# Kernel tuning notes

Measured on AMD Instinct MI355X. Metric: run time of the kernel, lower is better.

## Reference

```python
import jax, jax.numpy as jnp
import numpy as np

B, N, C, H, D, K = 4, 8192, 384, 12, 2, 256
M = N // K          # 32 members per cluster
CH = C // H         # 32 head dim


def setup_inputs() -> dict:
    key = jax.random.key(0)
    ks = jax.random.split(key, 8)
    pos = jax.random.uniform(ks[0], (B, N, D), jnp.float32) * 100.0
    feat = jax.random.normal(ks[1], (B, N, C), jnp.float32)
    # each batch's points partitioned into K clusters of M members (a permutation)
    perms = jax.vmap(lambda kk: jax.random.permutation(kk, N))(jax.random.split(ks[2], B))
    member_idx = perms.reshape(B * K, M).astype(jnp.int32)               # z x m
    batch_idx = jnp.broadcast_to(
        jnp.repeat(jnp.arange(B, dtype=jnp.int32), K)[:, None], (B * K, M))
    w = 0.02
    qkv_w = jax.random.normal(ks[3], (3 * C, C), jnp.float32) * w
    qkv_b = jnp.zeros((3 * C,), jnp.float32)
    pos_w = jax.random.normal(ks[4], (H, D), jnp.float32) * w
    pos_b = jnp.zeros((H,), jnp.float32)
    proj_w = jax.random.normal(ks[5], (C, C), jnp.float32) * w
    proj_b = jnp.zeros((C,), jnp.float32)
    return dict(pos=pos, feat=feat, member_idx=member_idx, batch_idx=batch_idx,
                qkv_w=qkv_w, qkv_b=qkv_b, pos_w=pos_w, pos_b=pos_b,
                proj_w=proj_w, proj_b=proj_b, k=K)


def reference(pos, feat, member_idx, batch_idx, qkv_w, qkv_b, pos_w, pos_b,
              proj_w, proj_b, k):
    # attend_means=True, mask=None, cluster_score=None, q_subsample_idx=None path
    b, n, c = feat.shape
    d = pos.shape[2]
    h = pos_w.shape[0]
    ch = c // h
    z, m = member_idx.shape
    scale = ch ** -0.5

    qkv = feat @ qkv_w.T + qkv_b            # b,n,3c
    q = qkv[..., :c]                        # b,n,c
    kv = qkv[..., c:]                       # b,n,2c

    pos_orig = pos
    pos_n = pos / jnp.max(pos.reshape(-1, d), axis=0)   # per-coordinate max norm

    # irregular gather of kv / pos per cluster member
    kv_g = kv[batch_idx, member_idx]        # z,m,2c
    pos_g = pos_n[batch_idx, member_idx]    # z,m,d

    # cluster_score=None, mask=None -> uniform weights 1/m (mean over members)
    kv_mean = jnp.mean(kv_g, axis=1).reshape(b, k, 2, h, ch)
    pos_mean = jnp.mean(pos_g, axis=1).reshape(b, k, d)

    key_ = kv_mean[:, :, 0].transpose(0, 2, 1, 3)   # b,h,k,ch
    v = kv_mean[:, :, 1].transpose(0, 2, 1, 3)      # b,h,k,ch
    qh = q.reshape(b, n, h, ch).transpose(0, 2, 1, 3) * scale  # b,h,n,ch

    attn = jnp.einsum('bhnc,bhkc->bhnk', qh, key_)  # b,h,n,k
    rel_pos = pos_mean[:, None, :, :] - pos_orig[:, :, None, :]  # b,n,k,d
    pos_bias = jnp.einsum('bnkd,hd->bhnk', rel_pos, pos_w) + pos_b[None, :, None, None]
    attn = jax.nn.softmax(attn + pos_bias, axis=-1)

    out = jnp.einsum('bhnk,bhkc->bnhc', attn, v).reshape(b, n, c)
    return out @ proj_w.T + proj_b
```

## Files before the change

### kernel.cpp

```cpp
#include <hip/hip_runtime.h>

typedef __attribute__((ext_vector_type(8))) short bf16x8;
typedef __attribute__((ext_vector_type(4))) float f32x4;

#define MFMA16(a,b,c) __builtin_amdgcn_mfma_f32_16x16x32_bf16((a),(b),(c),0,0,0)

__device__ __forceinline__ float b2f(unsigned short u){
  union { unsigned u; float f; } x; x.u = ((unsigned)u) << 16; return x.f;
}
__device__ __forceinline__ unsigned short f2b(float f){
  union { float f; unsigned u; } x; x.f = f;
  unsigned r = x.u + 0x7FFFu + ((x.u >> 16) & 1u);
  return (unsigned short)(r >> 16);
}
__device__ __forceinline__ unsigned pk_rne(float a, float b){
  unsigned ua = __float_as_uint(a), ub = __float_as_uint(b);
  ua += 0x7FFFu + ((ua >> 16) & 1u);
  ub += 0x7FFFu + ((ub >> 16) & 1u);
  return __builtin_amdgcn_perm(ub, ua, 0x07060302u);
}
__device__ __forceinline__ unsigned pk_trunc(float a, float b){
  return __builtin_amdgcn_perm(__float_as_uint(b), __float_as_uint(a), 0x07060302u);
}
__device__ __forceinline__ bf16x8 mk8(unsigned a, unsigned b, unsigned c, unsigned d){
  union { uint4 u; bf16x8 h; } x; x.u = make_uint4(a,b,c,d); return x.h;
}
__device__ __forceinline__ int permp(int cl){
  return (cl & 0xE0) | (((cl >> 2) & 3) << 3) | (((cl >> 4) & 1) << 2) | (cl & 3);
}

typedef __attribute__((address_space(3))) unsigned int lds_u32;
typedef const __attribute__((address_space(1))) unsigned int glb_u32;
__device__ __forceinline__ void gl_lds16(const void* g, void* l){
  __builtin_amdgcn_global_load_lds((glb_u32*)g, (lds_u32*)l, 16, 0, 0);
}

__global__ __launch_bounds__(256) void cvt_kernel(const float* __restrict__ in,
                                                  unsigned short* __restrict__ o, long n8){
  long i = (long)blockIdx.x*256 + threadIdx.x;
  if (i >= n8) return;
  const float4* p = (const float4*)(in + i*8);
  float4 a = p[0], b = p[1];
  *(uint4*)(o + i*8) = make_uint4(pk_rne(a.x,a.y), pk_rne(a.z,a.w),
                                  pk_rne(b.x,b.y), pk_rne(b.z,b.w));
}

__global__ __launch_bounds__(256) void posmax_kernel(const float* __restrict__ pos,
                                                     unsigned* __restrict__ pmax){
  int i = blockIdx.x*256 + threadIdx.x;
  float4 v = ((const float4*)pos)[i];
  float m0 = fmaxf(v.x, v.z), m1 = fmaxf(v.y, v.w);
  #pragma unroll
  for (int off = 32; off >= 1; off >>= 1){
    m0 = fmaxf(m0, __shfl_xor(m0, off, 64));
    m1 = fmaxf(m1, __shfl_xor(m1, off, 64));
  }
  if ((threadIdx.x & 63) == 0){
    atomicMax(&pmax[0], __float_as_uint(m0));
    atomicMax(&pmax[1], __float_as_uint(m1));
  }
}

__global__ __launch_bounds__(192) void cluster_means_kernel(
    const float* __restrict__ feat, const float* __restrict__ pos,
    const int* __restrict__ member_idx, const int* __restrict__ batch_idx,
    unsigned short* __restrict__ fm, float* __restrict__ pm)
{
  int t = threadIdx.x;
  int g = t / 96, tl = t - g*96;
  int z = blockIdx.x*2 + g;
  __shared__ int bases[2][32];
  if (tl < 32) bases[g][tl] = batch_idx[z*32 + tl]*8192 + member_idx[z*32 + tl];
  __syncthreads();
  float4 a = {0.f,0.f,0.f,0.f};
  float p = 0.f;
  const float4* f4 = (const float4*)feat;
  #pragma unroll 4
  for (int m = 0; m < 32; m++){
    int row = bases[g][m];
    float4 v = f4[(long)row*96 + tl];
    a.x += v.x; a.y += v.y; a.z += v.z; a.w += v.w;
    if (tl < 2) p += pos[(long)row*2 + tl];
  }
  unsigned d0 = pk_rne(a.x*(1.f/32.f), a.y*(1.f/32.f));
  unsigned d1 = pk_rne(a.z*(1.f/32.f), a.w*(1.f/32.f));
  *(uint2*)(fm + (long)z*384 + tl*4) = make_uint2(d0, d1);
  if (tl < 2) pm[z*2 + tl] = p * (1.f/32.f);
}

__global__ __launch_bounds__(256) void bias_kernel(
    const float* __restrict__ pm, const float* __restrict__ pmaxf,
    const float* __restrict__ pos_w, const float* __restrict__ pos_b,
    unsigned short* __restrict__ wt)
{
  int idx = blockIdx.x*256 + threadIdx.x;
  int kc = idx & 255;
  int bh = idx >> 8;
  int h = bh % 12;
  float p0 = pm[((bh/12)*256 + kc)*2]   / pmaxf[0];
  float p1 = pm[((bh/12)*256 + kc)*2+1] / pmaxf[1];
  float bias = p0*pos_w[h*2] + p1*pos_w[h*2+1] + pos_b[h];
  wt[(bh << 8) + permp(kc)] = f2b(exp2f(bias * 1.44269504088896340f));
}

__global__ __launch_bounds__(256) void gemm_kv_kernel(
    const unsigned short* __restrict__ A, const unsigned short* __restrict__ W,
    const float* __restrict__ bias, unsigned short* __restrict__ kh,
    unsigned short* __restrict__ vt, const unsigned short* __restrict__ wt)
{
  __shared__ unsigned short As[64*64];
  __shared__ unsigned short Ws[128*64];
  const int N = 768, K = 384;
  int mt = blockIdx.x / 6, nt = blockIdx.x - mt*6;
  int m0 = mt << 6, n0 = nt << 7;
  int tid = threadIdx.x;
  int lane = tid & 63, wave = tid >> 6;
  int wr = (wave >> 1) << 5, wc = (wave & 1) << 6;
  int l15 = lane & 15, quad = lane >> 4;
  int sw = l15 & 7;
  int srow = tid >> 3, sc8 = tid & 7;

  f32x4 acc[2][4];
  #pragma unroll
  for (int i = 0; i < 2; i++)
    #pragma unroll
    for (int j = 0; j < 4; j++) acc[i][j] = (f32x4){0.f,0.f,0.f,0.f};

  for (int k0 = 0; k0 < K; k0 += 64){
    __syncthreads();
    #pragma unroll
    for (int it = 0; it < 2; it++){
      int r = srow + it*32;
      int gc8 = sc8 ^ (r & 7);
      gl_lds16(A + (long)(m0+r)*K + k0 + gc8*8, As + it*2048 + wave*512);
    }
    #pragma unroll
    for (int it = 0; it < 4; it++){
      int r = srow + it*32;
      int gc8 = sc8 ^ (r & 7);
      gl_lds16(W + (long)(n0+r)*K + k0 + gc8*8, Ws + it*2048 + wave*512);
    }
    __syncthreads();
    #pragma unroll
    for (int kk = 0; kk < 2; kk++){
      bf16x8 af[2], bfr[4];
      #pragma unroll
      for (int i = 0; i < 2; i++)
        af[i] = *(const bf16x8*)(As + (wr + i*16 + l15)*64 + (((kk<<2)+quad) ^ sw)*8);
      #pragma unroll
      for (int j = 0; j < 4; j++)
        bfr[j] = *(const bf16x8*)(Ws + (wc + j*16 + l15)*64 + (((kk<<2)+quad) ^ sw)*8);
      #pragma unroll
      for (int i = 0; i < 2; i++)
        #pragma unroll
        for (int j = 0; j < 4; j++)
          acc[i][j] = MFMA16(af[i], bfr[j], acc[i][j]);
    }
  }

  #pragma unroll
  for (int j = 0; j < 4; j++){
    int col = n0 + wc + j*16 + l15;
    float bv = bias[col];
    #pragma unroll
    for (int i = 0; i < 2; i++){
      int row0 = m0 + wr + i*16 + quad*4;
      #pragma unroll
      for (int r = 0; r < 4; r++){
        float v = acc[i][j][r] + bv;
        int row = row0 + r;
        int b = row >> 8, cl = row & 255;
        if (col < 384){
          int h = col >> 5, ch = col & 31;
          kh[((((long)b*12 + h)*256 + cl)*32) + ch] = f2b(v);
        } else {
          int cn = col - 384;
          int h = cn >> 5, ch = cn & 31;
          int pp = permp(cl);
          int c8 = (pp >> 3) ^ (ch & 7);
          float w = b2f(wt[(((long)b*12 + h) << 8) + pp]);
          vt[(((long)b*12 + h)*32 + ch)*256 + c8*8 + (pp & 7)] = f2b(v * w);
        }
      }
    }
  }
}

template<int OUT_F32, int AF32>
__global__ __launch_bounds__(512) void gemm_fn_kernel(
    const void* __restrict__ Av, const unsigned short* __restrict__ W,
    const float* __restrict__ bias, void* __restrict__ Cv, float out_scale)
{
  __shared__ unsigned short As[64*72];
  __shared__ unsigned short Ws[384*64];
  const int K = 384, N = 384;
  int m0 = blockIdx.x << 6;
  int tid = threadIdx.x;
  int lane = tid & 63, wave = tid >> 6;
  int l15 = lane & 15, quad = lane >> 4;
  int sw = l15 & 7;
  int srow = tid >> 3, sc8 = tid & 7;

  f32x4 acc[4][3];
  #pragma unroll
  for (int i = 0; i < 4; i++)
    #pragma unroll
    for (int j = 0; j < 3; j++) acc[i][j] = (f32x4){0.f,0.f,0.f,0.f};

  for (int k0 = 0; k0 < K; k0 += 64){
    __syncthreads();
    if (AF32){
      const float* Af = (const float*)Av;
      const float4* src = (const float4*)(Af + (long)(m0+srow)*K + k0 + sc8*8);
      float4 v0 = src[0], v1 = src[1];
      *(uint4*)(As + srow*72 + sc8*8) = make_uint4(pk_rne(v0.x,v0.y), pk_rne(v0.z,v0.w),
                                                   pk_rne(v1.x,v1.y), pk_rne(v1.z,v1.w));
    } else {
      const unsigned short* A = (const unsigned short*)Av;
      int gc8 = sc8 ^ (srow & 7);
      gl_lds16(A + (long)(m0+srow)*K + k0 + gc8*8, As + wave*512);
    }
    #pragma unroll
    for (int it = 0; it < 6; it++){
      int r = it*64 + srow;
      int gc8 = sc8 ^ (r & 7);
      gl_lds16(W + (long)r*K + k0 + gc8*8, Ws + it*4096 + wave*512);
    }
    __syncthreads();
    #pragma unroll
    for (int kk = 0; kk < 2; kk++){
      bf16x8 af[4];
      #pragma unroll
      for (int i = 0; i < 4; i++){
        int r = i*16 + l15;
        if (AF32) af[i] = *(const bf16x8*)(As + r*72 + ((kk<<2)+quad)*8);
        else      af[i] = *(const bf16x8*)(As + r*64 + (((kk<<2)+quad) ^ sw)*8);
      }
      #pragma unroll
      for (int j = 0; j < 3; j++){
        bf16x8 bfr = *(const bf16x8*)(Ws + (wave*48 + j*16 + l15)*64 + (((kk<<2)+quad) ^ sw)*8);
        #pragma unroll
        for (int i = 0; i < 4; i++)
          acc[i][j] = MFMA16(af[i], bfr, acc[i][j]);
      }
    }
  }

  #pragma unroll
  for (int j = 0; j < 3; j++){
    int col = wave*48 + j*16 + l15;
    float bv = bias[col];
    #pragma unroll
    for (int i = 0; i < 4; i++){
      int row0 = m0 + i*16 + quad*4;
      #pragma unroll
      for (int r = 0; r < 4; r++){
        float v = (acc[i][j][r] + bv) * out_scale;
        if (OUT_F32) ((float*)Cv)[(long)(row0+r)*N + col] = v;
        else ((unsigned short*)Cv)[(long)(row0+r)*N + col] = f2b(v);
      }
    }
  }
}

__global__ __launch_bounds__(256) void attn_kernel(
    const unsigned short* __restrict__ qs,
    const unsigned short* __restrict__ kh,
    const unsigned short* __restrict__ vt,
    const unsigned short* __restrict__ wt,
    unsigned short* __restrict__ ao)
{
  __shared__ unsigned short keyS[256*32];
  __shared__ unsigned short vTS[32*256];
  __shared__ unsigned short wS[256];

  int bid = blockIdx.x;
  int chunk = bid & 127;
  int h = (bid >> 7) % 12;
  int b = bid / (128*12);
  int bh = b*12 + h;
  int n0 = chunk << 6;
  int tid = threadIdx.x, lane = tid & 63, wave = tid >> 6;
  int l15 = lane & 15, quad = lane >> 4;
  int sw = l15 & 7;

  const unsigned short* khb = kh + (long)bh*8192;
  const unsigned short* vtb = vt + (long)bh*8192;
  #pragma unroll
  for (int it = 0; it < 4; it++){
    gl_lds16(khb + it*2048 + tid*8, keyS + it*2048 + wave*512);
    gl_lds16(vtb + it*2048 + tid*8, vTS  + it*2048 + wave*512);
  }
  if (tid < 32) *(uint4*)(wS + tid*8) = *(const uint4*)(wt + ((long)bh << 8) + tid*8);
  __syncthreads();

  int tok0 = n0 + wave*16;
  bf16x8 aq = *(const bf16x8*)(qs + ((long)b*8192 + tok0 + l15)*384 + h*32 + quad*8);

  f32x4 S[16];
  #pragma unroll
  for (int kb = 0; kb < 16; kb++){
    bf16x8 bk = *(const bf16x8*)(keyS + (kb*16 + l15)*32 + quad*8);
    f32x4 z = {0.f,0.f,0.f,0.f};
    S[kb] = MFMA16(bk, aq, z);
  }

  #pragma unroll
  for (int kb = 0; kb < 16; kb++)
    #pragma unroll
    for (int c = 0; c < 4; c++) S[kb][c] = exp2f(S[kb][c]);

  f32x4 o0 = {0.f,0.f,0.f,0.f}, o1 = {0.f,0.f,0.f,0.f}, os = {0.f,0.f,0.f,0.f};
  #pragma unroll
  for (int ks = 0; ks < 8; ks++){
    bf16x8 pf = mk8(pk_trunc(S[2*ks][0],   S[2*ks][1]),
                    pk_trunc(S[2*ks][2],   S[2*ks][3]),
                    pk_trunc(S[2*ks+1][0], S[2*ks+1][1]),
                    pk_trunc(S[2*ks+1][2], S[2*ks+1][3]));
    int c8 = (4*ks + quad) ^ sw;
    bf16x8 a0 = *(const bf16x8*)(vTS + l15*256      + c8*8);
    bf16x8 a1 = *(const bf16x8*)(vTS + (16+l15)*256 + c8*8);
    bf16x8 wf = *(const bf16x8*)(wS + ks*32 + quad*8);
    o0 = MFMA16(a0, pf, o0);
    o1 = MFMA16(a1, pf, o1);
    os = MFMA16(wf, pf, os);
  }
  float inv = 1.f / os[0];
  long obase = ((long)b*8192 + tok0 + l15)*384 + h*32 + quad*4;
  unsigned q0 = pk_rne(o0[0]*inv, o0[1]*inv), q1 = pk_rne(o0[2]*inv, o0[3]*inv);
  unsigned q2 = pk_rne(o1[0]*inv, o1[1]*inv), q3 = pk_rne(o1[2]*inv, o1[3]*inv);
  *(uint2*)(ao + obase)      = make_uint2(q0, q1);
  *(uint2*)(ao + obase + 16) = make_uint2(q2, q3);
}

extern "C" void kernel_launch(void* const* d_in, const int* in_sizes, int n_in,
                              void* d_out, int out_size, void* d_ws, size_t ws_size,
                              hipStream_t stream)
{
  const float* pos      = (const float*)d_in[0];
  const float* feat     = (const float*)d_in[1];
  const int* member_idx = (const int*)d_in[2];
  const int* batch_idx  = (const int*)d_in[3];
  const float* qkv_w    = (const float*)d_in[4];
  const float* qkv_b    = (const float*)d_in[5];
  const float* pos_w    = (const float*)d_in[6];
  const float* pos_b    = (const float*)d_in[7];
  const float* proj_w   = (const float*)d_in[8];
  const float* proj_b   = (const float*)d_in[9];
  float* out = (float*)d_out;

  char* ws = (char*)d_ws;
  float* pmax           = (float*)ws;
  float* pm             = (float*)(ws + 256);
  unsigned short* fm    = (unsigned short*)(ws + 8704);
  unsigned short* kh    = (unsigned short*)(ws + 795136);
  unsigned short* vt    = (unsigned short*)(ws + 1581568);
  unsigned short* wt    = (unsigned short*)(ws + 2368000);
  unsigned short* q_s   = (unsigned short*)(ws + 2417152);
  unsigned short* ao    = (unsigned short*)(ws + 27582976);
  unsigned short* qkvwb = (unsigned short*)(ws + 52748800);
  unsigned short* projwb= (unsigned short*)(ws + 53633536);

  hipMemsetAsync(pmax, 0, 8, stream);
  posmax_kernel<<<64, 256, 0, stream>>>(pos, (unsigned*)pmax);
  cvt_kernel<<<216, 256, 0, stream>>>(qkv_w, qkvwb, 55296);
  cvt_kernel<<<72, 256, 0, stream>>>(proj_w, projwb, 18432);
  cluster_means_kernel<<<512, 192, 0, stream>>>(feat, pos, member_idx, batch_idx, fm, pm);
  bias_kernel<<<48, 256, 0, stream>>>(pm, pmax, pos_w, pos_b, wt);
  gemm_kv_kernel<<<96, 256, 0, stream>>>(fm, qkvwb + 384*384, qkv_b + 384, kh, vt, wt);
  gemm_fn_kernel<0,1><<<512, 512, 0, stream>>>(feat, qkvwb, qkv_b, q_s,
                                               0.17677669529663687f * 1.44269504088896340f);
  attn_kernel<<<6144, 256, 0, stream>>>(q_s, kh, vt, wt, ao);
  gemm_fn_kernel<1,0><<<512, 512, 0, stream>>>(ao, projwb, proj_b, out, 1.0f);
}
```

Measured before the change: 224.8 us.

## Fuse prep kernels and restructure row GEMM to read weights from global

Merges the position-max reduction and the two weight-conversion kernels into one launch to save launch overhead. The row GEMM now stages the whole 64x384 A tile in LDS once and reads B fragments directly from global memory (L2-resident bf16 weights) instead of staging 384x64 weight slices each k-step. This drops the per-k-step barriers and cuts LDS use, which may raise occupancy. The cost is more global/L2 traffic per wave for the weight fragments. The cluster-means loop unroll also goes from 4 to 8.

```diff
diff --git a/kernel.cpp b/kernel.cpp
--- a/kernel.cpp
+++ b/kernel.cpp
@@ -35,29 +35,33 @@
   __builtin_amdgcn_global_load_lds((glb_u32*)g, (lds_u32*)l, 16, 0, 0);
 }
 
-__global__ __launch_bounds__(256) void cvt_kernel(const float* __restrict__ in,
-                                                  unsigned short* __restrict__ o, long n8){
-  long i = (long)blockIdx.x*256 + threadIdx.x;
-  if (i >= n8) return;
-  const float4* p = (const float4*)(in + i*8);
-  float4 a = p[0], b = p[1];
-  *(uint4*)(o + i*8) = make_uint4(pk_rne(a.x,a.y), pk_rne(a.z,a.w),
-                                  pk_rne(b.x,b.y), pk_rne(b.z,b.w));
-}
-
-__global__ __launch_bounds__(256) void posmax_kernel(const float* __restrict__ pos,
-                                                     unsigned* __restrict__ pmax){
-  int i = blockIdx.x*256 + threadIdx.x;
-  float4 v = ((const float4*)pos)[i];
-  float m0 = fmaxf(v.x, v.z), m1 = fmaxf(v.y, v.w);
-  #pragma unroll
-  for (int off = 32; off >= 1; off >>= 1){
-    m0 = fmaxf(m0, __shfl_xor(m0, off, 64));
-    m1 = fmaxf(m1, __shfl_xor(m1, off, 64));
-  }
-  if ((threadIdx.x & 63) == 0){
-    atomicMax(&pmax[0], __float_as_uint(m0));
-    atomicMax(&pmax[1], __float_as_uint(m1));
+__global__ __launch_bounds__(256) void prep_kernel(
+    const float* __restrict__ pos, unsigned* __restrict__ pmax,
+    const float* __restrict__ qkv_w, unsigned short* __restrict__ qkvwb,
+    const float* __restrict__ proj_w, unsigned short* __restrict__ projwb)
+{
+  int bid = blockIdx.x, tid = threadIdx.x;
+  if (bid < 64){
+    int i = bid*256 + tid;
+    float4 v = ((const float4*)pos)[i];
+    float m0 = fmaxf(v.x, v.z), m1 = fmaxf(v.y, v.w);
+    #pragma unroll
+    for (int off = 32; off >= 1; off >>= 1){
+      m0 = fmaxf(m0, __shfl_xor(m0, off, 64));
+      m1 = fmaxf(m1, __shfl_xor(m1, off, 64));
+    }
+    if ((tid & 63) == 0){
+      atomicMax(&pmax[0], __float_as_uint(m0));
+      atomicMax(&pmax[1], __float_as_uint(m1));
+    }
+  } else {
+    const float* in; unsigned short* o; long i;
+    if (bid < 280){ in = qkv_w;  o = qkvwb;  i = (long)(bid-64)*256 + tid; }
+    else          { in = proj_w; o = projwb; i = (long)(bid-280)*256 + tid; }
+    const float4* p = (const float4*)(in + i*8);
+    float4 a = p[0], b = p[1];
+    *(uint4*)(o + i*8) = make_uint4(pk_rne(a.x,a.y), pk_rne(a.z,a.w),
+                                    pk_rne(b.x,b.y), pk_rne(b.z,b.w));
   }
 }
 
@@ -75,7 +79,7 @@
   float4 a = {0.f,0.f,0.f,0.f};
   float p = 0.f;
   const float4* f4 = (const float4*)feat;
-  #pragma unroll 4
+  #pragma unroll 8
   for (int m = 0; m < 32; m++){
     int row = bases[g][m];
     float4 v = f4[(long)row*96 + tl];
@@ -191,15 +195,33 @@
     const void* __restrict__ Av, const unsigned short* __restrict__ W,
     const float* __restrict__ bias, void* __restrict__ Cv, float out_scale)
 {
-  __shared__ unsigned short As[64*72];
-  __shared__ unsigned short Ws[384*64];
+  __shared__ unsigned short As[6*64*64];
   const int K = 384, N = 384;
   int m0 = blockIdx.x << 6;
   int tid = threadIdx.x;
   int lane = tid & 63, wave = tid >> 6;
   int l15 = lane & 15, quad = lane >> 4;
-  int sw = l15 & 7;
-  int srow = tid >> 3, sc8 = tid & 7;
+  int sr = tid >> 3, sc8 = tid & 7;
+
+  if (AF32){
+    const float* Af = (const float*)Av;
+    #pragma unroll
+    for (int it = 0; it < 6; it++){
+      int gc = it*64 + (sc8 ^ (sr & 7))*8;
+      const float4* src = (const float4*)(Af + (long)(m0+sr)*K + gc);
+      float4 v0 = src[0], v1 = src[1];
+      *(uint4*)(As + it*4096 + sr*64 + sc8*8) =
+        make_uint4(pk_rne(v0.x,v0.y), pk_rne(v0.z,v0.w), pk_rne(v1.x,v1.y), pk_rne(v1.z,v1.w));
+    }
+  } else {
+    const unsigned short* A = (const unsigned short*)Av;
+    #pragma unroll
+    for (int it = 0; it < 6; it++){
+      int gc8 = sc8 ^ (sr & 7);
+      gl_lds16(A + (long)(m0+sr)*K + it*64 + gc8*8, As + it*4096 + wave*512);
+    }
+  }
+  __syncthreads();
 
   f32x4 acc[4][3];
   #pragma unroll
@@ -207,48 +229,29 @@
     #pragma unroll
     for (int j = 0; j < 3; j++) acc[i][j] = (f32x4){0.f,0.f,0.f,0.f};
 
-  for (int k0 = 0; k0 < K; k0 += 64){
-    __syncthreads();
-    if (AF32){
-      const float* Af = (const float*)Av;
-      const float4* src = (const float4*)(Af + (long)(m0+srow)*K + k0 + sc8*8);
-      float4 v0 = src[0], v1 = src[1];
-      *(uint4*)(As + srow*72 + sc8*8) = make_uint4(pk_rne(v0.x,v0.y), pk_rne(v0.z,v0.w),
-                                                   pk_rne(v1.x,v1.y), pk_rne(v1.z,v1.w));
-    } else {
-      const unsigned short* A = (const unsigned short*)Av;
-      int gc8 = sc8 ^ (srow & 7);
-      gl_lds16(A + (long)(m0+srow)*K + k0 + gc8*8, As + wave*512);
-    }
-    #pragma unroll
-    for (int it = 0; it < 6; it++){
-      int r = it*64 + srow;
-      int gc8 = sc8 ^ (r & 7);
-      gl_lds16(W + (long)r*K + k0 + gc8*8, Ws + it*4096 + wave*512);
-    }
-    __syncthreads();
-    #pragma unroll
-    for (int kk = 0; kk < 2; kk++){
-      bf16x8 af[4];
-      #pragma unroll
-      for (int i = 0; i < 4; i++){
-        int r = i*16 + l15;
-        if (AF32) af[i] = *(const bf16x8*)(As + r*72 + ((kk<<2)+quad)*8);
-        else      af[i] = *(const bf16x8*)(As + r*64 + (((kk<<2)+quad) ^ sw)*8);
-      }
-      #pragma unroll
-      for (int j = 0; j < 3; j++){
-        bf16x8 bfr = *(const bf16x8*)(Ws + (wave*48 + j*16 + l15)*64 + (((kk<<2)+quad) ^ sw)*8);
-        #pragma unroll
-        for (int i = 0; i < 4; i++)
-          acc[i][j] = MFMA16(af[i], bfr, acc[i][j]);
-      }
-    }
+  int n0w = wave*48;
+  #pragma unroll
+  for (int ks = 0; ks < 12; ks++){
+    int it = ks >> 1, cb = (ks & 1)*4;
+    bf16x8 af[4], bw[3];
+    #pragma unroll
+    for (int j = 0; j < 3; j++)
+      bw[j] = *(const bf16x8*)(W + (long)(n0w + j*16 + l15)*K + ks*32 + quad*8);
+    #pragma unroll
+    for (int i = 0; i < 4; i++){
+      int r = i*16 + l15;
+      af[i] = *(const bf16x8*)(As + it*4096 + r*64 + (((cb+quad) ^ (l15 & 7))*8));
+    }
+    #pragma unroll
+    for (int i = 0; i < 4; i++)
+      #pragma unroll
+      for (int j = 0; j < 3; j++)
+        acc[i][j] = MFMA16(af[i], bw[j], acc[i][j]);
   }
 
   #pragma unroll
   for (int j = 0; j < 3; j++){
-    int col = wave*48 + j*16 + l15;
+    int col = n0w + j*16 + l15;
     float bv = bias[col];
     #pragma unroll
     for (int i = 0; i < 4; i++){
@@ -362,9 +365,7 @@
   unsigned short* projwb= (unsigned short*)(ws + 53633536);
 
   hipMemsetAsync(pmax, 0, 8, stream);
-  posmax_kernel<<<64, 256, 0, stream>>>(pos, (unsigned*)pmax);
-  cvt_kernel<<<216, 256, 0, stream>>>(qkv_w, qkvwb, 55296);
-  cvt_kernel<<<72, 256, 0, stream>>>(proj_w, projwb, 18432);
+  prep_kernel<<<352, 256, 0, stream>>>(pos, (unsigned*)pmax, qkv_w, qkvwb, proj_w, projwb);
   cluster_means_kernel<<<512, 192, 0, stream>>>(feat, pos, member_idx, batch_idx, fm, pm);
   bias_kernel<<<48, 256, 0, stream>>>(pm, pmax, pos_w, pos_b, wt);
   gemm_kv_kernel<<<96, 256, 0, stream>>>(fm, qkvwb + 384*384, qkv_b + 384, kh, vt, wt);
```

Result: slower. 238.7 us (+6.2%).

## Use head-major Q and attention-output layouts, double attention work per block, fuse prep kernels

Applied to the files above, without the earlier changes.

The Q projection now writes its output in head-major (b,h,n,32) layout, and the output projection reads attention output from that layout. This gives the attention kernel contiguous 64-byte rows per token instead of strided 384-wide rows. Each attention block now handles 128 tokens (two 16-token tiles per wave), so key/value staging is amortized over twice the work and the grid is halved. The pos-max and two weight-conversion kernels are merged into one launch, and the cluster-means loop unroll is raised. The cost is scattered 2-byte stores in the Q GEMM epilogue and gathered loads in the proj GEMM, plus fewer blocks in the attention grid.

```diff
diff --git a/kernel.cpp b/kernel.cpp
--- a/kernel.cpp
+++ b/kernel.cpp
@@ -35,29 +35,33 @@
   __builtin_amdgcn_global_load_lds((glb_u32*)g, (lds_u32*)l, 16, 0, 0);
 }
 
-__global__ __launch_bounds__(256) void cvt_kernel(const float* __restrict__ in,
-                                                  unsigned short* __restrict__ o, long n8){
-  long i = (long)blockIdx.x*256 + threadIdx.x;
-  if (i >= n8) return;
-  const float4* p = (const float4*)(in + i*8);
-  float4 a = p[0], b = p[1];
-  *(uint4*)(o + i*8) = make_uint4(pk_rne(a.x,a.y), pk_rne(a.z,a.w),
-                                  pk_rne(b.x,b.y), pk_rne(b.z,b.w));
-}
-
-__global__ __launch_bounds__(256) void posmax_kernel(const float* __restrict__ pos,
-                                                     unsigned* __restrict__ pmax){
-  int i = blockIdx.x*256 + threadIdx.x;
-  float4 v = ((const float4*)pos)[i];
-  float m0 = fmaxf(v.x, v.z), m1 = fmaxf(v.y, v.w);
-  #pragma unroll
-  for (int off = 32; off >= 1; off >>= 1){
-    m0 = fmaxf(m0, __shfl_xor(m0, off, 64));
-    m1 = fmaxf(m1, __shfl_xor(m1, off, 64));
-  }
-  if ((threadIdx.x & 63) == 0){
-    atomicMax(&pmax[0], __float_as_uint(m0));
-    atomicMax(&pmax[1], __float_as_uint(m1));
+__global__ __launch_bounds__(256) void prep_kernel(
+    const float* __restrict__ pos, unsigned* __restrict__ pmax,
+    const float* __restrict__ qkv_w, unsigned short* __restrict__ qkvwb,
+    const float* __restrict__ proj_w, unsigned short* __restrict__ projwb)
+{
+  int bid = blockIdx.x, tid = threadIdx.x;
+  if (bid < 64){
+    int i = bid*256 + tid;
+    float4 v = ((const float4*)pos)[i];
+    float m0 = fmaxf(v.x, v.z), m1 = fmaxf(v.y, v.w);
+    #pragma unroll
+    for (int off = 32; off >= 1; off >>= 1){
+      m0 = fmaxf(m0, __shfl_xor(m0, off, 64));
+      m1 = fmaxf(m1, __shfl_xor(m1, off, 64));
+    }
+    if ((tid & 63) == 0){
+      atomicMax(&pmax[0], __float_as_uint(m0));
+      atomicMax(&pmax[1], __float_as_uint(m1));
+    }
+  } else {
+    const float* in; unsigned short* o; long i;
+    if (bid < 280){ in = qkv_w;  o = qkvwb;  i = (long)(bid-64)*256 + tid; }
+    else          { in = proj_w; o = projwb; i = (long)(bid-280)*256 + tid; }
+    const float4* p = (const float4*)(in + i*8);
+    float4 a = p[0], b = p[1];
+    *(uint4*)(o + i*8) = make_uint4(pk_rne(a.x,a.y), pk_rne(a.z,a.w),
+                                    pk_rne(b.x,b.y), pk_rne(b.z,b.w));
   }
 }
 
@@ -75,7 +79,7 @@
   float4 a = {0.f,0.f,0.f,0.f};
   float p = 0.f;
   const float4* f4 = (const float4*)feat;
-  #pragma unroll 4
+  #pragma unroll 8
   for (int m = 0; m < 32; m++){
     int row = bases[g][m];
     float4 v = f4[(long)row*96 + tl];
@@ -186,7 +190,7 @@
   }
 }
 
-template<int OUT_F32, int AF32>
+template<int OUT_F32, int AF32, int AHM, int CHM>
 __global__ __launch_bounds__(512) void gemm_fn_kernel(
     const void* __restrict__ Av, const unsigned short* __restrict__ W,
     const float* __restrict__ bias, void* __restrict__ Cv, float out_scale)
@@ -218,7 +222,16 @@
     } else {
       const unsigned short* A = (const unsigned short*)Av;
       int gc8 = sc8 ^ (srow & 7);
-      gl_lds16(A + (long)(m0+srow)*K + k0 + gc8*8, As + wave*512);
+      const unsigned short* src;
+      if (AHM){
+        int row = m0 + srow;
+        int bb = row >> 13, tok = row & 8191;
+        int ch = k0 + gc8*8;
+        src = A + ((((long)(bb*12 + (ch >> 5))) << 13) + tok)*32 + (ch & 31);
+      } else {
+        src = A + (long)(m0+srow)*K + k0 + gc8*8;
+      }
+      gl_lds16(src, As + wave*512);
     }
     #pragma unroll
     for (int it = 0; it < 6; it++){
@@ -256,30 +269,35 @@
       #pragma unroll
       for (int r = 0; r < 4; r++){
         float v = (acc[i][j][r] + bv) * out_scale;
-        if (OUT_F32) ((float*)Cv)[(long)(row0+r)*N + col] = v;
-        else ((unsigned short*)Cv)[(long)(row0+r)*N + col] = f2b(v);
+        int row = row0 + r;
+        if (OUT_F32){
+          ((float*)Cv)[(long)row*N + col] = v;
+        } else if (CHM){
+          int bb = row >> 13, tok = row & 8191;
+          ((unsigned short*)Cv)[((((long)(bb*12 + (col >> 5))) << 13) + tok)*32 + (col & 31)] = f2b(v);
+        } else {
+          ((unsigned short*)Cv)[(long)row*N + col] = f2b(v);
+        }
       }
     }
   }
 }
 
 __global__ __launch_bounds__(256) void attn_kernel(
-    const unsigned short* __restrict__ qs,
+    const unsigned short* __restrict__ qhm,
     const unsigned short* __restrict__ kh,
     const unsigned short* __restrict__ vt,
     const unsigned short* __restrict__ wt,
-    unsigned short* __restrict__ ao)
+    unsigned short* __restrict__ aohm)
 {
   __shared__ unsigned short keyS[256*32];
   __shared__ unsigned short vTS[32*256];
   __shared__ unsigned short wS[256];
 
   int bid = blockIdx.x;
-  int chunk = bid & 127;
-  int h = (bid >> 7) % 12;
-  int b = bid / (128*12);
-  int bh = b*12 + h;
-  int n0 = chunk << 6;
+  int chunk = bid & 63;
+  int bh = bid >> 6;
+  int n0 = chunk << 7;
   int tid = threadIdx.x, lane = tid & 63, wave = tid >> 6;
   int l15 = lane & 15, quad = lane >> 4;
   int sw = l15 & 7;
@@ -292,45 +310,51 @@
     gl_lds16(vtb + it*2048 + tid*8, vTS  + it*2048 + wave*512);
   }
   if (tid < 32) *(uint4*)(wS + tid*8) = *(const uint4*)(wt + ((long)bh << 8) + tid*8);
+
+  long qbase = ((long)bh*8192 + n0 + wave*32 + l15)*32 + quad*8;
+  bf16x8 aq0 = *(const bf16x8*)(qhm + qbase);
+  bf16x8 aq1 = *(const bf16x8*)(qhm + qbase + 512);
   __syncthreads();
 
-  int tok0 = n0 + wave*16;
-  bf16x8 aq = *(const bf16x8*)(qs + ((long)b*8192 + tok0 + l15)*384 + h*32 + quad*8);
-
-  f32x4 S[16];
-  #pragma unroll
-  for (int kb = 0; kb < 16; kb++){
-    bf16x8 bk = *(const bf16x8*)(keyS + (kb*16 + l15)*32 + quad*8);
-    f32x4 z = {0.f,0.f,0.f,0.f};
-    S[kb] = MFMA16(bk, aq, z);
-  }
-
-  #pragma unroll
-  for (int kb = 0; kb < 16; kb++)
-    #pragma unroll
-    for (int c = 0; c < 4; c++) S[kb][c] = exp2f(S[kb][c]);
-
-  f32x4 o0 = {0.f,0.f,0.f,0.f}, o1 = {0.f,0.f,0.f,0.f}, os = {0.f,0.f,0.f,0.f};
-  #pragma unroll
-  for (int ks = 0; ks < 8; ks++){
-    bf16x8 pf = mk8(pk_trunc(S[2*ks][0],   S[2*ks][1]),
-                    pk_trunc(S[2*ks][2],   S[2*ks][3]),
-                    pk_trunc(S[2*ks+1][0], S[2*ks+1][1]),
-                    pk_trunc(S[2*ks+1][2], S[2*ks+1][3]));
-    int c8 = (4*ks + quad) ^ sw;
-    bf16x8 a0 = *(const bf16x8*)(vTS + l15*256      + c8*8);
-    bf16x8 a1 = *(const bf16x8*)(vTS + (16+l15)*256 + c8*8);
-    bf16x8 wf = *(const bf16x8*)(wS + ks*32 + quad*8);
-    o0 = MFMA16(a0, pf, o0);
-    o1 = MFMA16(a1, pf, o1);
-    os = MFMA16(wf, pf, os);
-  }
-  float inv = 1.f / os[0];
-  long obase = ((long)b*8192 + tok0 + l15)*384 + h*32 + quad*4;
-  unsigned q0 = pk_rne(o0[0]*inv, o0[1]*inv), q1 = pk_rne(o0[2]*inv, o0[3]*inv);
-  unsigned q2 = pk_rne(o1[0]*inv, o1[1]*inv), q3 = pk_rne(o1[2]*inv, o1[3]*inv);
-  *(uint2*)(ao + obase)      = make_uint2(q0, q1);
-  *(uint2*)(ao + obase + 16) = make_uint2(q2, q3);
+  #pragma unroll
+  for (int ti = 0; ti < 2; ti++){
+    bf16x8 aq = ti ? aq1 : aq0;
+
+    f32x4 S[16];
+    #pragma unroll
+    for (int kb = 0; kb < 16; kb++){
+      bf16x8 bk = *(const bf16x8*)(keyS + (kb*16 + l15)*32 + quad*8);
+      f32x4 z = {0.f,0.f,0.f,0.f};
+      S[kb] = MFMA16(bk, aq, z);
+    }
+
+    #pragma unroll
+    for (int kb = 0; kb < 16; kb++)
+      #pragma unroll
+      for (int c = 0; c < 4; c++) S[kb][c] = exp2f(S[kb][c]);
+
+    f32x4 o0 = {0.f,0.f,0.f,0.f}, o1 = {0.f,0.f,0.f,0.f}, os = {0.f,0.f,0.f,0.f};
+    #pragma unroll
+    for (int ks = 0; ks < 8; ks++){
+      bf16x8 pf = mk8(pk_trunc(S[2*ks][0],   S[2*ks][1]),
+                      pk_trunc(S[2*ks][2],   S[2*ks][3]),
+                      pk_trunc(S[2*ks+1][0], S[2*ks+1][1]),
+                      pk_trunc(S[2*ks+1][2], S[2*ks+1][3]));
+      int c8 = (4*ks + quad) ^ sw;
+      bf16x8 a0 = *(const bf16x8*)(vTS + l15*256      + c8*8);
+      bf16x8 a1 = *(const bf16x8*)(vTS + (16+l15)*256 + c8*8);
+      bf16x8 wf = *(const bf16x8*)(wS + ks*32 + quad*8);
+      o0 = MFMA16(a0, pf, o0);
+      o1 = MFMA16(a1, pf, o1);
+      os = MFMA16(wf, pf, os);
+    }
+    float inv = 1.f / os[0];
+    long obase = ((long)bh*8192 + n0 + wave*32 + ti*16 + l15)*32 + quad*4;
+    unsigned q0 = pk_rne(o0[0]*inv, o0[1]*inv), q1 = pk_rne(o0[2]*inv, o0[3]*inv);
+    unsigned q2 = pk_rne(o1[0]*inv, o1[1]*inv), q3 = pk_rne(o1[2]*inv, o1[3]*inv);
+    *(uint2*)(aohm + obase)      = make_uint2(q0, q1);
+    *(uint2*)(aohm + obase + 16) = make_uint2(q2, q3);
+  }
 }
 
 extern "C" void kernel_launch(void* const* d_in, const int* in_sizes, int n_in,
@@ -362,14 +386,12 @@
   unsigned short* projwb= (unsigned short*)(ws + 53633536);
 
   hipMemsetAsync(pmax, 0, 8, stream);
-  posmax_kernel<<<64, 256, 0, stream>>>(pos, (unsigned*)pmax);
-  cvt_kernel<<<216, 256, 0, stream>>>(qkv_w, qkvwb, 55296);
-  cvt_kernel<<<72, 256, 0, stream>>>(proj_w, projwb, 18432);
+  prep_kernel<<<352, 256, 0, stream>>>(pos, (unsigned*)pmax, qkv_w, qkvwb, proj_w, projwb);
   cluster_means_kernel<<<512, 192, 0, stream>>>(feat, pos, member_idx, batch_idx, fm, pm);
   bias_kernel<<<48, 256, 0, stream>>>(pm, pmax, pos_w, pos_b, wt);
   gemm_kv_kernel<<<96, 256, 0, stream>>>(fm, qkvwb + 384*384, qkv_b + 384, kh, vt, wt);
-  gemm_fn_kernel<0,1><<<512, 512, 0, stream>>>(feat, qkvwb, qkv_b, q_s,
-                                               0.17677669529663687f * 1.44269504088896340f);
-  attn_kernel<<<6144, 256, 0, stream>>>(q_s, kh, vt, wt, ao);
-  gemm_fn_kernel<1,0><<<512, 512, 0, stream>>>(ao, projwb, proj_b, out, 1.0f);
-}
+  gemm_fn_kernel<0,1,0,1><<<512, 512, 0, stream>>>(feat, qkvwb, qkv_b, q_s,
+                                                   0.17677669529663687f * 1.44269504088896340f);
+  attn_kernel<<<3072, 256, 0, stream>>>(q_s, kh, vt, wt, ao);
+  gemm_fn_kernel<1,0,1,0><<<512, 512, 0, stream>>>(ao, projwb, proj_b, out, 1.0f);
+}
```

New measurement: 217.9 us. 1.03x faster.
